# Optimization experiments

Hardware: AMD Instinct MI355X
Metric: run time of the kernel (lower is better)

## Reference

```python
import jax, jax.numpy as jnp
import numpy as np

POOL = 16  # in_downsampling == internal_downsampling == 16


def _conv1x1(x, w, b):
    # x: [B,C,H,W], w: [O,C], b: [O] -> [B,O,H,W]
    return jnp.einsum('oc,bchw->bohw', w, x) + b[None, :, None, None]


def _maxpool(x, k):
    return jax.lax.reduce_window(x, -jnp.inf, jax.lax.max,
                                 (1, 1, k, k), (1, 1, k, k), 'VALID')


def setup_inputs() -> dict:
    key = jax.random.key(0)
    ks = jax.random.split(key, 7)
    B, C, Ci, H, W = 4, 256, 128, 256, 256
    s_in = 1.0 / np.sqrt(C)
    return {
        'x':   jax.random.normal(ks[0], (B, C, H, W), jnp.float32),
        'f_w': jax.random.normal(ks[1], (Ci, C), jnp.float32) * s_in,
        'f_b': jax.random.normal(ks[2], (Ci,), jnp.float32) * 0.01,
        'g_w': jax.random.normal(ks[3], (Ci, C), jnp.float32) * s_in,
        'g_b': jax.random.normal(ks[4], (Ci,), jnp.float32) * 0.01,
        'h_w': jax.random.normal(ks[5], (C, C), jnp.float32) * s_in,
        'h_b': jax.random.normal(ks[6], (C,), jnp.float32) * 0.01,
    }


def reference(x, f_w, f_b, g_w, g_b, h_w, h_b):
    B, C, H, W = x.shape
    # pooled query / key features: [B, Ci, h1, w1] and [B, Ci, h2, w2]
    fv = _maxpool(_conv1x1(x, f_w, f_b), POOL)
    gv = _maxpool(_conv1x1(x, g_w, g_b), POOL)
    # dots[b,i,j,k,l] = sum_c fv[b,c,i,j] * gv[b,c,k,l]  (channel dot-product)
    dots = jnp.einsum('bcij,bckl->bijkl', fv, gv)
    Bd, h1, w1, h2, w2 = dots.shape
    # exp=True path: softmax over the flattened (h2, w2) key positions
    dots = jax.nn.softmax(dots.reshape(Bd, h1, w1, h2 * w2), axis=-1)
    dots = dots.reshape(Bd, h1, w1, h2, w2)
    # pooled values: [B, C, h2, w2]
    hv = _maxpool(_conv1x1(x, h_w, h_b), POOL)
    # weighted sum over key positions -> [B, C, h1, w1]
    out = jnp.einsum('bijkl,bckl->bcij', dots, hv)
    # bilinear upsample (align_corners=False == half-pixel, matches jax resize)
    up = jax.image.resize(out, (B, C, H, W), method='bilinear')
    return up + x
```

## Files before the change

### kernel.cpp

```cpp
#include <hip/hip_runtime.h>
#include <hip/hip_fp16.h>

typedef _Float16 f16;
typedef _Float16 f16x4_t __attribute__((ext_vector_type(4)));
typedef _Float16 f16x8_t __attribute__((ext_vector_type(8)));
typedef float    f32x4_t __attribute__((ext_vector_type(4)));

#define NB  4
#define NC  256
#define NH  256
#define NW  256

__global__ __launch_bounds__(256) void k_convert_w(
    const float* __restrict__ f_w, const float* __restrict__ g_w,
    const float* __restrict__ h_w, f16* __restrict__ wf)
{
    int id = blockIdx.x * 256 + threadIdx.x;
    int cout = id >> 8;
    float v;
    if (cout < 128)       v = f_w[id];
    else if (cout < 256)  v = g_w[id - 128*256];
    else                  v = h_w[id - 256*256];
    wf[id] = (f16)v;
}

__global__ __launch_bounds__(512, 2) void k_pooled_conv(
    const float* __restrict__ x, const f16* __restrict__ wf,
    const float* __restrict__ f_b, const float* __restrict__ g_b,
    const float* __restrict__ h_b,
    float* __restrict__ pooled_fg,
    float* __restrict__ pooledT_h)
{
    __shared__ __align__(16) char smem[65536];

    const int t    = threadIdx.x;
    const int wave = t >> 6;
    const int lane = t & 63;
    const int l15  = lane & 15;
    const int lg   = lane >> 4;
    const bool isfg = (wave < 4);
    const int coutbase = wave * 64;

    f16x8_t bfrag[4][8];
    #pragma unroll
    for (int n = 0; n < 4; n++) {
        const f16* wr = wf + (coutbase + n*16 + l15) * 256 + lg*8;
        #pragma unroll
        for (int k = 0; k < 8; k++)
            bfrag[n][k] = *(const f16x8_t*)(wr + k*32);
    }
    float biasv[4];
    #pragma unroll
    for (int n = 0; n < 4; n++) {
        int c = coutbase + n*16 + l15;
        biasv[n] = (c < 128) ? f_b[c] : (c < 256) ? g_b[c - 128] : h_b[c - 256];
    }

    const int q   = t & 3;
    const int dyl = (t >> 2) & 1;
    const int c0  = (t >> 3) * 4;
    unsigned woff[4];
    #pragma unroll
    for (int w = 0; w < 4; w++) {
        int dx = q + 4*w;
        unsigned lslot = (unsigned)(dx | (((c0 >> 3) & 3) << 4));
        woff[w] = ((unsigned)(dyl*8 + (c0 >> 5)) << 10) + lslot*16u + (unsigned)((c0 & 4) * 2);
    }

    const int bid   = blockIdx.x;
    const int b     = bid >> 6;
    const int wbase = bid * 4;
    const float* xb = x + (size_t)b * (256u * 65536u);

    float vmax[4] = {-3.0e38f, -3.0e38f, -3.0e38f, -3.0e38f};

    auto loadst = [&](int gsd, float* r) {
        int win = wbase + (gsd >> 3);
        int s   = gsd & 7;
        int wi = (win >> 4) & 15, wj = win & 15;
        const float* src = xb + (size_t)c0 * 65536u
                         + (unsigned)((wi*16 + s*2 + dyl) * 256 + wj*16 + q);
        #pragma unroll
        for (int cc = 0; cc < 4; cc++)
            #pragma unroll
            for (int w = 0; w < 4; w++)
                r[cc*4 + w] = src[(unsigned)cc * 65536u + (unsigned)w * 4u];
    };
    auto writest = [&](const float* r, int buf) {
        char* base = smem + buf * 32768;
        #pragma unroll
        for (int w = 0; w < 4; w++) {
            f16x4_t hv, lv;
            #pragma unroll
            for (int cc = 0; cc < 4; cc++) {
                float v = r[cc*4 + w];
                f16 h = (f16)v;
                hv[cc] = h;
                lv[cc] = (f16)(v - (float)h);
            }
            *(f16x4_t*)(base + woff[w])         = hv;
            *(f16x4_t*)(base + 16384 + woff[w]) = lv;
        }
    };
    auto mfmast = [&](int buf) {
        const char* base = smem + buf * 32768 + lane * 16;
        #pragma unroll
        for (int m = 0; m < 2; m++) {
            f32x4_t acc[4] = {{0.f,0.f,0.f,0.f},{0.f,0.f,0.f,0.f},
                              {0.f,0.f,0.f,0.f},{0.f,0.f,0.f,0.f}};
            #pragma unroll
            for (int k = 0; k < 8; k++) {
                const char* p = base + ((m*8 + k) << 10);
                f16x8_t ah = *(const f16x8_t*)p;
                #pragma unroll
                for (int n = 0; n < 4; n++)
                    acc[n] = __builtin_amdgcn_mfma_f32_16x16x32_f16(ah, bfrag[n][k], acc[n], 0,0,0);
                if (isfg) {
                    f16x8_t al = *(const f16x8_t*)(p + 16384);
                    #pragma unroll
                    for (int n = 0; n < 4; n++)
                        acc[n] = __builtin_amdgcn_mfma_f32_16x16x32_f16(al, bfrag[n][k], acc[n], 0,0,0);
                }
            }
            #pragma unroll
            for (int n = 0; n < 4; n++)
                #pragma unroll
                for (int r = 0; r < 4; r++)
                    vmax[n] = fmaxf(vmax[n], acc[n][r]);
        }
    };
    auto finalize = [&](int win) {
        int wn = win & 255;
        #pragma unroll
        for (int n = 0; n < 4; n++) {
            float v = vmax[n];
            v = fmaxf(v, __shfl_xor(v, 16, 64));
            v = fmaxf(v, __shfl_xor(v, 32, 64));
            if (lane < 16) {
                float val = v + biasv[n];
                int c = coutbase + n*16 + lane;
                if (isfg) pooled_fg[((b*256 + c)  << 8) + wn] = val;
                else      pooledT_h[((b*256 + wn) << 8) + (c - 256)] = val;
            }
            vmax[n] = -3.0e38f;
        }
    };

    float rA[16], rB[16];
    loadst(0, rA);
    writest(rA, 0);
    loadst(1, rB);
    __syncthreads();

    #pragma unroll 1
    for (int gs = 0; gs < 32; gs += 2) {
        if (gs + 2 < 32) loadst(gs + 2, rA);
        writest(rB, 1);
        mfmast(0);
        __syncthreads();
        if (gs + 3 < 32) loadst(gs + 3, rB);
        if (gs + 2 < 32) writest(rA, 0);
        mfmast(1);
        if ((gs & 7) == 6) finalize(wbase + (gs >> 3));
        __syncthreads();
    }
}

__global__ __launch_bounds__(256) void k_attn(
    const float* __restrict__ pooled_fg, const float* __restrict__ pooledT_h,
    float* __restrict__ attnout)
{
    __shared__ float red[4];
    __shared__ float p_lds[256];
    const int blk = blockIdx.x;
    const int b = blk >> 8;
    const int q = blk & 255;
    const int t = threadIdx.x;

    const float* fv = pooled_fg + ((b*256) << 8) + q;
    const float* gv = pooled_fg + ((b*256 + 128) << 8) + t;

    float s = 0.f;
    #pragma unroll 8
    for (int c = 0; c < 128; c++)
        s += fv[c << 8] * gv[c << 8];

    float m = s;
    #pragma unroll
    for (int o = 1; o < 64; o <<= 1) m = fmaxf(m, __shfl_xor(m, o, 64));
    if ((t & 63) == 0) red[t >> 6] = m;
    __syncthreads();
    m = fmaxf(fmaxf(red[0], red[1]), fmaxf(red[2], red[3]));
    __syncthreads();

    float p = expf(s - m);
    float sum = p;
    #pragma unroll
    for (int o = 1; o < 64; o <<= 1) sum += __shfl_xor(sum, o, 64);
    if ((t & 63) == 0) red[t >> 6] = sum;
    __syncthreads();
    sum = red[0] + red[1] + red[2] + red[3];
    p /= sum;
    p_lds[t] = p;
    __syncthreads();

    const float* hv = pooledT_h + (b << 16) + t;
    float acc = 0.f;
    #pragma unroll 8
    for (int k = 0; k < 256; k++)
        acc += p_lds[k] * hv[k << 8];
    attnout[((b*256 + t) << 8) + q] = acc;
}

__global__ __launch_bounds__(256) void k_upsample_add(
    const float* __restrict__ x, const float* __restrict__ attnout,
    float* __restrict__ out)
{
    __shared__ float L[256];
    const int blk = blockIdx.x;
    const int t = threadIdx.x;
    L[t] = attnout[(blk << 8) + t];
    __syncthreads();
    const float* xp = x   + (size_t)blk * 65536;
    float*       op = out + (size_t)blk * 65536;

    const int x4 = (t & 63) << 2;
    const int yo = t >> 6;
    float fxv[4]; int x0v[4], x1v[4];
    #pragma unroll
    for (int e = 0; e < 4; e++) {
        float sx  = (x4 + e + 0.5f) * 0.0625f - 0.5f;
        float x0f = floorf(sx);
        fxv[e] = sx - x0f;
        int ix0 = (int)x0f;
        x0v[e] = min(15, max(0, ix0));
        x1v[e] = min(15, max(0, ix0 + 1));
    }
    for (int it = 0; it < 64; it++) {
        int y = it*4 + yo;
        float sy  = (y + 0.5f) * 0.0625f - 0.5f;
        float y0f = floorf(sy);
        float fy  = sy - y0f;
        int iy0 = (int)y0f;
        int y0 = min(15, max(0, iy0));
        int y1 = min(15, max(0, iy0 + 1));
        const float* Ly0 = L + y0*16;
        const float* Ly1 = L + y1*16;
        float4 xin = *(const float4*)(xp + y*256 + x4);
        float o[4]; const float* xe = (const float*)&xin;
        #pragma unroll
        for (int e = 0; e < 4; e++) {
            float top = Ly0[x0v[e]] + fxv[e] * (Ly0[x1v[e]] - Ly0[x0v[e]]);
            float bot = Ly1[x0v[e]] + fxv[e] * (Ly1[x1v[e]] - Ly1[x0v[e]]);
            o[e] = top + fy * (bot - top) + xe[e];
        }
        float4 ov = make_float4(o[0], o[1], o[2], o[3]);
        *(float4*)(op + y*256 + x4) = ov;
    }
}

extern "C" void kernel_launch(void* const* d_in, const int* in_sizes, int n_in,
                              void* d_out, int out_size, void* d_ws, size_t ws_size,
                              hipStream_t stream)
{
    const float* x   = (const float*)d_in[0];
    const float* f_w = (const float*)d_in[1];
    const float* f_b = (const float*)d_in[2];
    const float* g_w = (const float*)d_in[3];
    const float* g_b = (const float*)d_in[4];
    const float* h_w = (const float*)d_in[5];
    const float* h_b = (const float*)d_in[6];
    float* out = (float*)d_out;

    char* ws = (char*)d_ws;
    f16*   wf        = (f16*)ws;
    float* pooled_fg = (float*)(ws + (256<<10));
    float* pooledT_h = (float*)(ws + (256<<10) + (1<<20));
    float* attnout   = (float*)(ws + (256<<10) + (2<<20));

    k_convert_w   <<<512, 256, 0, stream>>>(f_w, g_w, h_w, wf);
    k_pooled_conv <<<256, 512, 0, stream>>>(x, wf, f_b, g_b, h_b, pooled_fg, pooledT_h);
    k_attn        <<<1024, 256, 0, stream>>>(pooled_fg, pooledT_h, attnout);
    k_upsample_add<<<1024, 256, 0, stream>>>(x, attnout, out);
}
```

Before: 305.9 us.

## Split pooled-conv output channels across twice as many waves per block

Blocks of the pooled 1x1-conv kernel grow from 512 to 1024 threads. Each wave now computes 32 output channels instead of 64. Each thread loads 8 channels at a single pixel instead of 4 channels at 4 pixels, and writes one f16x8 store per half to LDS. The goal is more waves per CU to hide the global-load latency of x, since the 256-block grid gives roughly one block per CU. In exchange, the (1024,4) launch bound may force a tight register budget and cause spills.

```diff
diff --git a/kernel.cpp b/kernel.cpp
--- a/kernel.cpp
+++ b/kernel.cpp
@@ -24,7 +24,7 @@
     wf[id] = (f16)v;
 }
 
-__global__ __launch_bounds__(512, 2) void k_pooled_conv(
+__global__ __launch_bounds__(1024, 4) void k_pooled_conv(
     const float* __restrict__ x, const f16* __restrict__ wf,
     const float* __restrict__ f_b, const float* __restrict__ g_b,
     const float* __restrict__ h_b,
@@ -38,101 +38,89 @@
     const int lane = t & 63;
     const int l15  = lane & 15;
     const int lg   = lane >> 4;
-    const bool isfg = (wave < 4);
-    const int coutbase = wave * 64;
-
-    f16x8_t bfrag[4][8];
-    #pragma unroll
-    for (int n = 0; n < 4; n++) {
+    const bool isfg = (wave < 8);
+    const int coutbase = isfg ? wave * 32 : 256 + (wave - 8) * 32;
+
+    f16x8_t bfrag[2][8];
+    #pragma unroll
+    for (int n = 0; n < 2; n++) {
         const f16* wr = wf + (coutbase + n*16 + l15) * 256 + lg*8;
         #pragma unroll
         for (int k = 0; k < 8; k++)
             bfrag[n][k] = *(const f16x8_t*)(wr + k*32);
     }
-    float biasv[4];
-    #pragma unroll
-    for (int n = 0; n < 4; n++) {
+    float biasv[2];
+    #pragma unroll
+    for (int n = 0; n < 2; n++) {
         int c = coutbase + n*16 + l15;
         biasv[n] = (c < 128) ? f_b[c] : (c < 256) ? g_b[c - 128] : h_b[c - 256];
     }
 
-    const int q   = t & 3;
-    const int dyl = (t >> 2) & 1;
-    const int c0  = (t >> 3) * 4;
-    unsigned woff[4];
-    #pragma unroll
-    for (int w = 0; w < 4; w++) {
-        int dx = q + 4*w;
-        unsigned lslot = (unsigned)(dx | (((c0 >> 3) & 3) << 4));
-        woff[w] = ((unsigned)(dyl*8 + (c0 >> 5)) << 10) + lslot*16u + (unsigned)((c0 & 4) * 2);
-    }
+    const int dx  = t & 15;
+    const int dyl = (t >> 4) & 1;
+    const int c8  = (t >> 5) * 8;
+    const unsigned page = (unsigned)(dyl*8 + (c8 >> 5));
+    const unsigned slot = (unsigned)(dx | (((c8 >> 3) & 3) << 4));
+    const unsigned woff = (page << 10) + slot * 16u;
 
     const int bid   = blockIdx.x;
     const int b     = bid >> 6;
     const int wbase = bid * 4;
     const float* xb = x + (size_t)b * (256u * 65536u);
 
-    float vmax[4] = {-3.0e38f, -3.0e38f, -3.0e38f, -3.0e38f};
+    float vmax[2] = {-3.0e38f, -3.0e38f};
 
     auto loadst = [&](int gsd, float* r) {
         int win = wbase + (gsd >> 3);
         int s   = gsd & 7;
         int wi = (win >> 4) & 15, wj = win & 15;
-        const float* src = xb + (size_t)c0 * 65536u
-                         + (unsigned)((wi*16 + s*2 + dyl) * 256 + wj*16 + q);
-        #pragma unroll
-        for (int cc = 0; cc < 4; cc++)
-            #pragma unroll
-            for (int w = 0; w < 4; w++)
-                r[cc*4 + w] = src[(unsigned)cc * 65536u + (unsigned)w * 4u];
+        const float* src = xb + (size_t)c8 * 65536u
+                         + (unsigned)((wi*16 + s*2 + dyl) * 256 + wj*16 + dx);
+        #pragma unroll
+        for (int cc = 0; cc < 8; cc++)
+            r[cc] = src[(unsigned)cc * 65536u];
     };
     auto writest = [&](const float* r, int buf) {
         char* base = smem + buf * 32768;
-        #pragma unroll
-        for (int w = 0; w < 4; w++) {
-            f16x4_t hv, lv;
-            #pragma unroll
-            for (int cc = 0; cc < 4; cc++) {
-                float v = r[cc*4 + w];
-                f16 h = (f16)v;
-                hv[cc] = h;
-                lv[cc] = (f16)(v - (float)h);
-            }
-            *(f16x4_t*)(base + woff[w])         = hv;
-            *(f16x4_t*)(base + 16384 + woff[w]) = lv;
-        }
+        f16x8_t hv, lv;
+        #pragma unroll
+        for (int cc = 0; cc < 8; cc++) {
+            float v = r[cc];
+            f16 h = (f16)v;
+            hv[cc] = h;
+            lv[cc] = (f16)(v - (float)h);
+        }
+        *(f16x8_t*)(base + woff)         = hv;
+        *(f16x8_t*)(base + 16384 + woff) = lv;
     };
     auto mfmast = [&](int buf) {
         const char* base = smem + buf * 32768 + lane * 16;
         #pragma unroll
         for (int m = 0; m < 2; m++) {
-            f32x4_t acc[4] = {{0.f,0.f,0.f,0.f},{0.f,0.f,0.f,0.f},
-                              {0.f,0.f,0.f,0.f},{0.f,0.f,0.f,0.f}};
+            f32x4_t acc0 = {0.f,0.f,0.f,0.f}, acc1 = {0.f,0.f,0.f,0.f};
             #pragma unroll
             for (int k = 0; k < 8; k++) {
                 const char* p = base + ((m*8 + k) << 10);
                 f16x8_t ah = *(const f16x8_t*)p;
-                #pragma unroll
-                for (int n = 0; n < 4; n++)
-                    acc[n] = __builtin_amdgcn_mfma_f32_16x16x32_f16(ah, bfrag[n][k], acc[n], 0,0,0);
+                acc0 = __builtin_amdgcn_mfma_f32_16x16x32_f16(ah, bfrag[0][k], acc0, 0,0,0);
+                acc1 = __builtin_amdgcn_mfma_f32_16x16x32_f16(ah, bfrag[1][k], acc1, 0,0,0);
                 if (isfg) {
                     f16x8_t al = *(const f16x8_t*)(p + 16384);
-                    #pragma unroll
-                    for (int n = 0; n < 4; n++)
-                        acc[n] = __builtin_amdgcn_mfma_f32_16x16x32_f16(al, bfrag[n][k], acc[n], 0,0,0);
+                    acc0 = __builtin_amdgcn_mfma_f32_16x16x32_f16(al, bfrag[0][k], acc0, 0,0,0);
+                    acc1 = __builtin_amdgcn_mfma_f32_16x16x32_f16(al, bfrag[1][k], acc1, 0,0,0);
                 }
             }
             #pragma unroll
-            for (int n = 0; n < 4; n++)
-                #pragma unroll
-                for (int r = 0; r < 4; r++)
-                    vmax[n] = fmaxf(vmax[n], acc[n][r]);
+            for (int r = 0; r < 4; r++) {
+                vmax[0] = fmaxf(vmax[0], acc0[r]);
+                vmax[1] = fmaxf(vmax[1], acc1[r]);
+            }
         }
     };
     auto finalize = [&](int win) {
         int wn = win & 255;
         #pragma unroll
-        for (int n = 0; n < 4; n++) {
+        for (int n = 0; n < 2; n++) {
             float v = vmax[n];
             v = fmaxf(v, __shfl_xor(v, 16, 64));
             v = fmaxf(v, __shfl_xor(v, 32, 64));
@@ -146,7 +134,7 @@
         }
     };
 
-    float rA[16], rB[16];
+    float rA[8], rB[8];
     loadst(0, rA);
     writest(rA, 0);
     loadst(1, rB);
@@ -279,7 +267,7 @@
     float* attnout   = (float*)(ws + (256<<10) + (2<<20));
 
     k_convert_w   <<<512, 256, 0, stream>>>(f_w, g_w, h_w, wf);
-    k_pooled_conv <<<256, 512, 0, stream>>>(x, wf, f_b, g_b, h_b, pooled_fg, pooledT_h);
+    k_pooled_conv <<<256, 1024, 0, stream>>>(x, wf, f_b, g_b, h_b, pooled_fg, pooledT_h);
     k_attn        <<<1024, 256, 0, stream>>>(pooled_fg, pooledT_h, attnout);
     k_upsample_add<<<1024, 256, 0, stream>>>(x, attnout, out);
 }
```

Result: faster. 296.1 us (-3.2%).
